# Optimization experiments

Measured on AMD Instinct MI355X. Metric: run time of the kernel, lower is better.

Reference implementation:

```python
import jax, jax.numpy as jnp
import numpy as np

EMBEDDING_DIM = 10
CONTEXT_SIZE_1 = 1
CONTEXT_SIZE_2 = 3
VOCAB = 50000
N = 1_000_000
NUM_NUMERIC = 16


def setup_inputs() -> dict:
    key = jax.random.key(0)
    ks = jax.random.split(key, 9)
    text_1 = jax.random.randint(ks[0], (N,), 0, VOCAB)
    text_2 = jax.random.randint(ks[1], (N,), 0, VOCAB)
    numeric_features = jax.random.normal(ks[2], (N, NUM_NUMERIC), dtype=jnp.float32)
    emb_table_1 = jax.random.normal(ks[3], (VOCAB, EMBEDDING_DIM), dtype=jnp.float32)
    emb_table_2 = jax.random.normal(ks[4], (VOCAB, EMBEDDING_DIM), dtype=jnp.float32)
    d_in = 2 * EMBEDDING_DIM + NUM_NUMERIC
    W1 = jax.random.normal(ks[5], (d_in, 128), dtype=jnp.float32) / np.sqrt(d_in)
    b1 = jnp.zeros((128,), dtype=jnp.float32)
    W2 = jax.random.normal(ks[6], (128, 1), dtype=jnp.float32) / np.sqrt(128.0)
    b2 = jnp.zeros((1,), dtype=jnp.float32)
    return {
        "text_1": text_1,
        "text_2": text_2,
        "numeric_features": numeric_features,
        "emb_table_1": emb_table_1,
        "emb_table_2": emb_table_2,
        "W1": W1,
        "b1": b1,
        "W2": W2,
        "b2": b2,
    }


def _contextual_embedding(ids, table, context_size):
    # mean of embeddings over window [i-cs, i+cs], clipped at sequence edges
    n = ids.shape[0]
    emb = table[ids]  # [N, D] gather
    # prefix sums with leading zero row: S[j] = sum(emb[0:j])
    S = jnp.concatenate([jnp.zeros((1, emb.shape[1]), emb.dtype),
                         jnp.cumsum(emb, axis=0)], axis=0)
    pos = jnp.arange(n)
    lo = jnp.maximum(pos - context_size, 0)
    hi = jnp.minimum(pos + context_size + 1, n)
    wsum = S[hi] - S[lo]                       # [N, D]
    count = (hi - lo).astype(emb.dtype)[:, None]
    return wsum / count


def reference(text_1, text_2, numeric_features, emb_table_1, emb_table_2, W1, b1, W2, b2):
    embed_1 = _contextual_embedding(text_1, emb_table_1, CONTEXT_SIZE_1)  # [N, 10]
    embed_2 = _contextual_embedding(text_2, emb_table_2, CONTEXT_SIZE_2)  # [N, 10]
    combined = jnp.concatenate([embed_1, embed_2, numeric_features], axis=1)
    h = jax.nn.relu(combined @ W1 + b1)
    out = h @ W2 + b2
    return jax.nn.sigmoid(out)  # [N, 1]
```

## Files before the change

### kernel.cpp

```cpp
#include <hip/hip_runtime.h>
#include <hip/hip_bf16.h>

#define EMB 10
#define DIN 36
#define HID 128
#define BM  128

typedef __attribute__((ext_vector_type(8))) short short8;
typedef __attribute__((ext_vector_type(4))) float f32x4;

__device__ __forceinline__ short bf16_hi(float v) {
  __hip_bfloat16 h = __float2bfloat16(v);
  return *reinterpret_cast<short*>(&h);
}
__device__ __forceinline__ float bf16_to_f(short s) {
  __hip_bfloat16 h = *reinterpret_cast<__hip_bfloat16*>(&s);
  return __bfloat162float(h);
}

__global__ void prep_kernel(const float* __restrict__ W1, const float* __restrict__ b1,
                            short* __restrict__ Bpack) {
  int b = blockIdx.x;
  int term = b >> 4;
  int ct   = (b >> 1) & 7;
  int ks   = b & 1;
  int l = threadIdx.x;
  int col = ct * 16 + (l & 15);
  int kb  = ks * 32 + (l >> 4) * 8;
  short8 o;
#pragma unroll
  for (int e = 0; e < 8; ++e) {
    int k = kb + e;
    float v = 0.0f;
    if (k < DIN)       v = W1[k * HID + col];
    else if (k == DIN) v = b1[col];
    short hb = bf16_hi(v);
    o[e] = (term == 0) ? hb : bf16_hi(v - bf16_to_f(hb));
  }
  *(short8*)(Bpack + (size_t)(((term * 8 + ct) * 2 + ks) * 64 + l) * 8) = o;
}

__global__ __launch_bounds__(256, 4)
void fused_kernel(const int* __restrict__ t1, const int* __restrict__ t2,
                  const float* __restrict__ numf,
                  const float* __restrict__ tab1, const float* __restrict__ tab2,
                  const short* __restrict__ Bpack,
                  const float* __restrict__ W2, const float* __restrict__ b2,
                  float* __restrict__ out, int N) {
  __shared__ float E1[BM + 2][11];
  __shared__ float E2[BM + 6][11];
  __shared__ float Cs[BM][38];
  __shared__ float W2s[HID];

  const int tid = threadIdx.x;
  const long base = (long)blockIdx.x * BM;
  const long row = base + tid;
  const bool rv = (tid < BM) && (row < (long)N);

  float4 nf0, nf1, nf2, nf3;
  if (rv) {
    const float4* np = (const float4*)(numf + row * 16);
    nf0 = np[0]; nf1 = np[1]; nf2 = np[2]; nf3 = np[3];
  }
  if (tid < BM + 2) {
    long g = base - 1 + tid;
    if (g >= 0 && g < N) {
      const float2* src = (const float2*)(tab1 + (long)t1[g] * EMB);
#pragma unroll
      for (int i = 0; i < 5; ++i) {
        float2 v = src[i];
        E1[tid][2 * i] = v.x; E1[tid][2 * i + 1] = v.y;
      }
    }
  }
  {
    int h = tid - (256 - (BM + 6));
    if (h >= 0) {
      long g = base - 3 + h;
      if (g >= 0 && g < N) {
        const float2* src = (const float2*)(tab2 + (long)t2[g] * EMB);
#pragma unroll
        for (int i = 0; i < 5; ++i) {
          float2 v = src[i];
          E2[h][2 * i] = v.x; E2[h][2 * i + 1] = v.y;
        }
      }
    }
  }
  if (tid >= 128) W2s[tid - 128] = W2[tid - 128];
  __syncthreads();

  if (rv) {
    float c[DIN + 1];
    {
      float s[EMB] = {0,0,0,0,0,0,0,0,0,0};
      int cnt = 0;
#pragma unroll
      for (int d = 0; d < 3; ++d) {
        long g = row - 1 + d;
        if (g >= 0 && g < N) {
          int h = tid + d;
#pragma unroll
          for (int i = 0; i < EMB; ++i) s[i] += E1[h][i];
          ++cnt;
        }
      }
      float inv = 1.0f / (float)cnt;
#pragma unroll
      for (int i = 0; i < EMB; ++i) c[i] = s[i] * inv;
    }
    {
      float s[EMB] = {0,0,0,0,0,0,0,0,0,0};
      int cnt = 0;
#pragma unroll
      for (int d = 0; d < 7; ++d) {
        long g = row - 3 + d;
        if (g >= 0 && g < N) {
          int h = tid + d;
#pragma unroll
          for (int i = 0; i < EMB; ++i) s[i] += E2[h][i];
          ++cnt;
        }
      }
      float inv = 1.0f / (float)cnt;
#pragma unroll
      for (int i = 0; i < EMB; ++i) c[EMB + i] = s[i] * inv;
    }
    c[20] = nf0.x; c[21] = nf0.y; c[22] = nf0.z; c[23] = nf0.w;
    c[24] = nf1.x; c[25] = nf1.y; c[26] = nf1.z; c[27] = nf1.w;
    c[28] = nf2.x; c[29] = nf2.y; c[30] = nf2.z; c[31] = nf2.w;
    c[32] = nf3.x; c[33] = nf3.y; c[34] = nf3.z; c[35] = nf3.w;
    c[DIN] = 1.0f;

#pragma unroll
    for (int k = 0; k <= DIN; ++k) Cs[tid][k] = c[k];
    Cs[tid][37] = 0.0f;
  }
  __syncthreads();

  const int wid = tid >> 6;
  const int l = tid & 63;
  const int arow = l & 15;
  const int kg = l >> 4;

  short8 aHi[2][2], aLo[2][2];
#pragma unroll
  for (int rtl = 0; rtl < 2; ++rtl) {
    const int r = (wid * 2 + rtl) * 16 + arow;
    const float* crow = &Cs[r][0];
    {
      float v[8];
#pragma unroll
      for (int i = 0; i < 4; ++i) {
        float2 t = *(const float2*)(crow + kg * 8 + 2 * i);
        v[2 * i] = t.x; v[2 * i + 1] = t.y;
      }
#pragma unroll
      for (int e = 0; e < 8; ++e) {
        short hb = bf16_hi(v[e]);
        aHi[rtl][0][e] = hb;
        aLo[rtl][0][e] = bf16_hi(v[e] - bf16_to_f(hb));
      }
    }
    if (kg == 0) {
      float v[8];
#pragma unroll
      for (int i = 0; i < 3; ++i) {
        float2 t = *(const float2*)(crow + 32 + 2 * i);
        v[2 * i] = t.x; v[2 * i + 1] = t.y;
      }
      v[6] = 0.0f; v[7] = 0.0f;
#pragma unroll
      for (int e = 0; e < 8; ++e) {
        short hb = bf16_hi(v[e]);
        aHi[rtl][1][e] = hb;
        aLo[rtl][1][e] = bf16_hi(v[e] - bf16_to_f(hb));
      }
    } else {
#pragma unroll
      for (int e = 0; e < 8; ++e) { aHi[rtl][1][e] = 0; aLo[rtl][1][e] = 0; }
    }
  }

  float part[2][4] = {{0,0,0,0},{0,0,0,0}};
#pragma unroll
  for (int ct = 0; ct < 8; ++ct) {
    short8 bb[2][2];
#pragma unroll
    for (int term = 0; term < 2; ++term)
#pragma unroll
      for (int ks = 0; ks < 2; ++ks)
        bb[term][ks] = *(const short8*)(Bpack +
            (size_t)(((term * 8 + ct) * 2 + ks) * 64 + l) * 8);
    float w2c = W2s[ct * 16 + (l & 15)];
#pragma unroll
    for (int rtl = 0; rtl < 2; ++rtl) {
      f32x4 acc = {0.0f, 0.0f, 0.0f, 0.0f};
#pragma unroll
      for (int ks = 0; ks < 2; ++ks) {
        acc = __builtin_amdgcn_mfma_f32_16x16x32_bf16(aHi[rtl][ks], bb[0][ks], acc, 0, 0, 0);
        acc = __builtin_amdgcn_mfma_f32_16x16x32_bf16(aLo[rtl][ks], bb[0][ks], acc, 0, 0, 0);
        acc = __builtin_amdgcn_mfma_f32_16x16x32_bf16(aHi[rtl][ks], bb[1][ks], acc, 0, 0, 0);
      }
#pragma unroll
      for (int r = 0; r < 4; ++r) {
        float hv = fmaxf(acc[r], 0.0f);
        part[rtl][r] += hv * w2c;
      }
    }
  }
#pragma unroll
  for (int off = 1; off < 16; off <<= 1) {
#pragma unroll
    for (int rtl = 0; rtl < 2; ++rtl)
#pragma unroll
      for (int r = 0; r < 4; ++r)
        part[rtl][r] += __shfl_xor(part[rtl][r], off, 64);
  }
  if ((l & 15) < 4) {
    float b2v = b2[0];
#pragma unroll
    for (int rtl = 0; rtl < 2; ++rtl) {
      int rt = wid * 2 + rtl;
      long grow = base + rt * 16 + (l >> 4) * 4 + (l & 15);
      if (grow < N) {
        float x = part[rtl][l & 15] + b2v;
        out[grow] = 1.0f / (1.0f + expf(-x));
      }
    }
  }
}

extern "C" void kernel_launch(void* const* d_in, const int* in_sizes, int n_in,
                              void* d_out, int out_size, void* d_ws, size_t ws_size,
                              hipStream_t stream) {
  const int*   t1   = (const int*)d_in[0];
  const int*   t2   = (const int*)d_in[1];
  const float* numf = (const float*)d_in[2];
  const float* tab1 = (const float*)d_in[3];
  const float* tab2 = (const float*)d_in[4];
  const float* W1   = (const float*)d_in[5];
  const float* b1   = (const float*)d_in[6];
  const float* W2   = (const float*)d_in[7];
  const float* b2   = (const float*)d_in[8];
  float* out = (float*)d_out;
  const int N = in_sizes[0];
  short* Bpack = (short*)d_ws;

  hipLaunchKernelGGL(prep_kernel, dim3(32), dim3(64), 0, stream, W1, b1, Bpack);
  int nblk = (N + BM - 1) / BM;
  hipLaunchKernelGGL(fused_kernel, dim3(nblk), dim3(256), 0, stream,
                     t1, t2, numf, tab1, tab2, Bpack, W2, b2, out, N);
}
```

Measured before the change: 202.2 us.

## Spread window-mean and numeric staging across all threads with sliding sums

Window-mean computation is now split across all 256 threads. Each thread owns one embedding dimension for a group of rows and computes the 3-wide and 7-wide means, the 7-wide one with a running sliding-window sum, instead of 128 threads each summing full windows. Numeric-feature loads are split into two halves across both thread halves, out-of-range embedding rows are zero-filled so the summation needs no bounds checks, and the occupancy hint in launch bounds is dropped. This aims to cut per-thread ALU and register pressure in the staging phase. In exchange it adds strided LDS column reads and some edge-case divisor logic.

```diff
diff --git a/kernel.cpp b/kernel.cpp
--- a/kernel.cpp
+++ b/kernel.cpp
@@ -40,7 +40,7 @@
   *(short8*)(Bpack + (size_t)(((term * 8 + ct) * 2 + ks) * 64 + l) * 8) = o;
 }
 
-__global__ __launch_bounds__(256, 4)
+__global__ __launch_bounds__(256)
 void fused_kernel(const int* __restrict__ t1, const int* __restrict__ t2,
                   const float* __restrict__ numf,
                   const float* __restrict__ tab1, const float* __restrict__ tab2,
@@ -54,87 +54,109 @@
 
   const int tid = threadIdx.x;
   const long base = (long)blockIdx.x * BM;
-  const long row = base + tid;
-  const bool rv = (tid < BM) && (row < (long)N);
-
-  float4 nf0, nf1, nf2, nf3;
-  if (rv) {
-    const float4* np = (const float4*)(numf + row * 16);
-    nf0 = np[0]; nf1 = np[1]; nf2 = np[2]; nf3 = np[3];
-  }
+  const int rloc = tid & 127;
+  const int half = tid >> 7;
+  const long rowm = base + rloc;
+
+  float4 nfa, nfb;
+  if (rowm < (long)N) {
+    const float4* np = (const float4*)(numf + rowm * 16 + half * 8);
+    nfa = np[0]; nfb = np[1];
+  }
+
   if (tid < BM + 2) {
     long g = base - 1 + tid;
-    if (g >= 0 && g < N) {
+    if (g >= 0 && g < (long)N) {
       const float2* src = (const float2*)(tab1 + (long)t1[g] * EMB);
 #pragma unroll
       for (int i = 0; i < 5; ++i) {
         float2 v = src[i];
         E1[tid][2 * i] = v.x; E1[tid][2 * i + 1] = v.y;
       }
+    } else {
+#pragma unroll
+      for (int i = 0; i < EMB; ++i) E1[tid][i] = 0.0f;
     }
   }
   {
     int h = tid - (256 - (BM + 6));
     if (h >= 0) {
       long g = base - 3 + h;
-      if (g >= 0 && g < N) {
+      if (g >= 0 && g < (long)N) {
         const float2* src = (const float2*)(tab2 + (long)t2[g] * EMB);
 #pragma unroll
         for (int i = 0; i < 5; ++i) {
           float2 v = src[i];
           E2[h][2 * i] = v.x; E2[h][2 * i + 1] = v.y;
         }
-      }
-    }
-  }
-  if (tid >= 128) W2s[tid - 128] = W2[tid - 128];
+      } else {
+#pragma unroll
+        for (int i = 0; i < EMB; ++i) E2[h][i] = 0.0f;
+      }
+    }
+  }
+  if (tid < HID) W2s[tid] = W2[tid];
   __syncthreads();
 
-  if (rv) {
-    float c[DIN + 1];
-    {
-      float s[EMB] = {0,0,0,0,0,0,0,0,0,0};
-      int cnt = 0;
-#pragma unroll
-      for (int d = 0; d < 3; ++d) {
-        long g = row - 1 + d;
-        if (g >= 0 && g < N) {
-          int h = tid + d;
-#pragma unroll
-          for (int i = 0; i < EMB; ++i) s[i] += E1[h][i];
-          ++cnt;
+  if (tid < 120) {
+    int grp = tid / 10, d = tid - grp * 10;
+    int r0 = grp * 11;
+    float e[13];
+#pragma unroll
+    for (int i = 0; i < 13; ++i) {
+      int h = r0 + i; if (h > 129) h = 129;
+      e[i] = E1[h][d];
+    }
+#pragma unroll
+    for (int i = 0; i < 11; ++i) {
+      int rr = r0 + i;
+      if (rr < BM) {
+        long row = base + rr;
+        float inv = 1.0f / 3.0f;
+        if (row == 0 || row >= (long)N - 1) {
+          long lo = row - 1; if (lo < 0) lo = 0;
+          long hi = row + 2; if (hi > (long)N) hi = (long)N;
+          long c = hi - lo;  if (c < 1) c = 1;
+          inv = 1.0f / (float)c;
         }
-      }
-      float inv = 1.0f / (float)cnt;
-#pragma unroll
-      for (int i = 0; i < EMB; ++i) c[i] = s[i] * inv;
-    }
-    {
-      float s[EMB] = {0,0,0,0,0,0,0,0,0,0};
-      int cnt = 0;
-#pragma unroll
-      for (int d = 0; d < 7; ++d) {
-        long g = row - 3 + d;
-        if (g >= 0 && g < N) {
-          int h = tid + d;
-#pragma unroll
-          for (int i = 0; i < EMB; ++i) s[i] += E2[h][i];
-          ++cnt;
+        Cs[rr][d] = (e[i] + e[i + 1] + e[i + 2]) * inv;
+      }
+    }
+  } else if (tid < 250) {
+    int u = tid - 120;
+    int grp = u / 10, d = u - grp * 10;
+    int r0 = grp * 10;
+    float e[16];
+#pragma unroll
+    for (int i = 0; i < 16; ++i) {
+      int h = r0 + i; if (h > 133) h = 133;
+      e[i] = E2[h][d];
+    }
+    float w = e[0] + e[1] + e[2] + e[3] + e[4] + e[5] + e[6];
+#pragma unroll
+    for (int i = 0; i < 10; ++i) {
+      int rr = r0 + i;
+      if (rr < BM) {
+        long row = base + rr;
+        float inv = 1.0f / 7.0f;
+        if (row < 3 || row >= (long)N - 3) {
+          long lo = row - 3; if (lo < 0) lo = 0;
+          long hi = row + 4; if (hi > (long)N) hi = (long)N;
+          long c = hi - lo;  if (c < 1) c = 1;
+          inv = 1.0f / (float)c;
         }
-      }
-      float inv = 1.0f / (float)cnt;
-#pragma unroll
-      for (int i = 0; i < EMB; ++i) c[EMB + i] = s[i] * inv;
-    }
-    c[20] = nf0.x; c[21] = nf0.y; c[22] = nf0.z; c[23] = nf0.w;
-    c[24] = nf1.x; c[25] = nf1.y; c[26] = nf1.z; c[27] = nf1.w;
-    c[28] = nf2.x; c[29] = nf2.y; c[30] = nf2.z; c[31] = nf2.w;
-    c[32] = nf3.x; c[33] = nf3.y; c[34] = nf3.z; c[35] = nf3.w;
-    c[DIN] = 1.0f;
-
-#pragma unroll
-    for (int k = 0; k <= DIN; ++k) Cs[tid][k] = c[k];
-    Cs[tid][37] = 0.0f;
+        Cs[rr][10 + d] = w * inv;
+      }
+      if (i < 9) w += e[i + 7] - e[i];
+    }
+  }
+  if (rowm < (long)N) {
+    float* cp = &Cs[rloc][20 + half * 8];
+    *(float2*)(cp + 0) = make_float2(nfa.x, nfa.y);
+    *(float2*)(cp + 2) = make_float2(nfa.z, nfa.w);
+    *(float2*)(cp + 4) = make_float2(nfb.x, nfb.y);
+    *(float2*)(cp + 6) = make_float2(nfb.z, nfb.w);
+    if (half == 0) *(float2*)(&Cs[rloc][36]) = make_float2(1.0f, 0.0f);
   }
   __syncthreads();
 
@@ -223,7 +245,7 @@
     for (int rtl = 0; rtl < 2; ++rtl) {
       int rt = wid * 2 + rtl;
       long grow = base + rt * 16 + (l >> 4) * 4 + (l & 15);
-      if (grow < N) {
+      if (grow < (long)N) {
         float x = part[rtl][l & 15] + b2v;
         out[grow] = 1.0f / (1.0f + expf(-x));
       }
```

Result: faster. 182.1 us (-9.9%).
